# Kernel optimization log

Hardware: AMD Instinct MI355X
Metric: run time of the kernel (lower is better)

## Reference

```python
import jax, jax.numpy as jnp
import numpy as np

FP8_MAX = 448.0  # e4m3fn max
ACT_EPS = 1e-4
W_EPS = 1e-6
BLK = 128


def quant_dequant_act_1x128(x):
    # x: [E, M, K]. One scale per (row, 128-col) tile; scale = max(|x|, eps)/448.
    E, M, K = x.shape
    xb = x.reshape(E, M, K // BLK, BLK)
    amax = jnp.max(jnp.abs(xb), axis=-1, keepdims=True)
    safe = jnp.maximum(amax, ACT_EPS)
    q = (xb * (FP8_MAX / safe)).astype(jnp.float8_e4m3fn)
    return (q.astype(jnp.float32) * (safe / FP8_MAX)).reshape(E, M, K)


def quant_dequant_weight_128x128(w):
    # w: [E, N, K]. One scale per 128x128 block; scale = max(|w|, eps)/448.
    E, N, K = w.shape
    wb = w.reshape(E, N // BLK, BLK, K // BLK, BLK)
    amax = jnp.max(jnp.abs(wb), axis=(2, 4), keepdims=True)
    safe = jnp.maximum(amax, W_EPS)
    q = (wb * (FP8_MAX / safe)).astype(jnp.float8_e4m3fn)
    return (q.astype(jnp.float32) * (safe / FP8_MAX)).reshape(E, N, K)


def setup_inputs() -> dict:
    key = jax.random.key(0)
    kx, kw = jax.random.split(key)
    E, M, K, N = 8, 4096, 2048, 2048
    x = jax.random.normal(kx, (E, M, K), dtype=jnp.float32)
    weight = jax.random.normal(kw, (E, N, K), dtype=jnp.float32) * 0.02
    return {"x": x, "weight": weight}


def reference(x, weight):
    # fp8 blockwise quantize both operands, then grouped GEMM per expert.
    xq = quant_dequant_act_1x128(x)          # [E, M, K]
    wq = quant_dequant_weight_128x128(weight)  # [E, N, K]
    return jnp.einsum('emk,enk->emn', xq, wq)  # [E, M, N]
```

## Files before the change

kernel.cpp:

```cpp
#include <hip/hip_runtime.h>

typedef float f32x4 __attribute__((ext_vector_type(4)));

static constexpr int E_ = 8, M_ = 4096, K_ = 2048, N_ = 2048;
static constexpr int KB_ = K_ / 128;
static constexpr int MT_ = M_ / 128;
static constexpr int NT_ = N_ / 128;
#define FP8MAX 448.0f

__global__ __launch_bounds__(256) void quant_x_kernel(const float* __restrict__ x,
                                                      unsigned char* __restrict__ qx,
                                                      float* __restrict__ sx) {
  long tile = (long)blockIdx.x * 8 + (threadIdx.x >> 5);
  int lane = threadIdx.x & 31;
  f32x4 v = *(const f32x4*)(x + tile * 128 + lane * 4);
  float am = fmaxf(fmaxf(fabsf(v[0]), fabsf(v[1])), fmaxf(fabsf(v[2]), fabsf(v[3])));
#pragma unroll
  for (int off = 16; off; off >>= 1) am = fmaxf(am, __shfl_xor(am, off, 32));
  float safe = fmaxf(am, 1e-4f);
  float qs = FP8MAX / safe;
  int pk = 0;
  pk = __builtin_amdgcn_cvt_pk_fp8_f32(v[0] * qs, v[1] * qs, pk, false);
  pk = __builtin_amdgcn_cvt_pk_fp8_f32(v[2] * qs, v[3] * qs, pk, true);
  *(int*)(qx + tile * 128 + lane * 4) = pk;
  if (lane == 0) sx[tile] = safe / FP8MAX;
}

__global__ __launch_bounds__(256) void quant_w_kernel(const float* __restrict__ w,
                                                      unsigned char* __restrict__ qw,
                                                      float* __restrict__ sw) {
  int b = blockIdx.x;
  int kb = b % KB_;
  int t2 = b / KB_;
  int nb = t2 % NT_;
  int e = t2 / NT_;
  int tid = threadIdx.x;
  int r = tid >> 1;
  int c0 = (tid & 1) * 64;
  const float* base = w + ((long)(e * N_ + nb * 128 + r)) * K_ + kb * 128 + c0;
  f32x4 v[16];
  float am = 0.f;
#pragma unroll
  for (int j = 0; j < 16; ++j) {
    v[j] = *(const f32x4*)(base + j * 4);
    am = fmaxf(am, fmaxf(fmaxf(fabsf(v[j][0]), fabsf(v[j][1])),
                         fmaxf(fabsf(v[j][2]), fabsf(v[j][3]))));
  }
#pragma unroll
  for (int off = 32; off; off >>= 1) am = fmaxf(am, __shfl_xor(am, off, 64));
  __shared__ float red[4];
  if ((tid & 63) == 0) red[tid >> 6] = am;
  __syncthreads();
  am = fmaxf(fmaxf(red[0], red[1]), fmaxf(red[2], red[3]));
  float safe = fmaxf(am, 1e-6f);
  float qs = FP8MAX / safe;
  unsigned char* outp = qw + ((long)(e * N_ + nb * 128 + r)) * K_ + kb * 128 + c0;
#pragma unroll
  for (int j4 = 0; j4 < 4; ++j4) {
    uint4 pkv;
    unsigned int* pp = (unsigned int*)&pkv;
#pragma unroll
    for (int q = 0; q < 4; ++q) {
      int j = j4 * 4 + q;
      int pk = 0;
      pk = __builtin_amdgcn_cvt_pk_fp8_f32(v[j][0] * qs, v[j][1] * qs, pk, false);
      pk = __builtin_amdgcn_cvt_pk_fp8_f32(v[j][2] * qs, v[j][3] * qs, pk, true);
      pp[q] = (unsigned int)pk;
    }
    *(uint4*)(outp + j4 * 16) = pkv;
  }
  if (tid == 0) sw[(e * NT_ + nb) * KB_ + kb] = safe / FP8MAX;
}

__device__ inline void gload_lds16(const void* g, void* l) {
  __builtin_amdgcn_global_load_lds(
      (const __attribute__((address_space(1))) unsigned int*)g,
      (__attribute__((address_space(3))) unsigned int*)l, 16, 0, 0);
}

__global__ __launch_bounds__(256, 2) void gemm_kernel(
    const unsigned char* __restrict__ qx, const unsigned char* __restrict__ qw,
    const float* __restrict__ sx, const float* __restrict__ sw,
    float* __restrict__ out) {
  __shared__ unsigned char As[128 * 128];
  __shared__ unsigned char Bs[128 * 128];
  __shared__ float sxl[128][17];
  __shared__ float swl[16];

  const int e = blockIdx.y;
  const int mt = blockIdx.x / NT_;
  const int nt = blockIdx.x % NT_;
  const int brow = mt * 128, bcol = nt * 128;
  const int tid = threadIdx.x;
  const int w = tid >> 6, l = tid & 63;
  const int wr = w >> 1, wc = w & 1;
  const int qq = l >> 4, rl = l & 15;

  {
    int row = tid >> 1, half = (tid & 1) * 8;
    const float* sp = sx + ((long)(e * M_ + brow + row)) * KB_ + half;
    f32x4 s0 = *(const f32x4*)sp;
    f32x4 s1 = *(const f32x4*)(sp + 4);
#pragma unroll
    for (int j = 0; j < 4; ++j) {
      sxl[row][half + j] = s0[j];
      sxl[row][half + 4 + j] = s1[j];
    }
    if (tid < KB_) swl[tid] = sw[(e * NT_ + nt) * KB_ + tid];
  }

  f32x4 acc[4][4] = {};

  const unsigned char* Ab = qx + (long)(e * M_ + brow) * K_;
  const unsigned char* Bb = qw + (long)(e * N_ + bcol) * K_;
  const int lr8 = l >> 3, lc8 = l & 7;
  const int sch = (lc8 ^ lr8) * 16;
  const int o8 = (qq & 1) * 8;
  const int ch = qq >> 1;

  for (int kb = 0; kb < KB_; ++kb) {
    __syncthreads();
#pragma unroll
    for (int i = 0; i < 4; ++i) {
      const int rt = i * 32 + w * 8;
      gload_lds16(Ab + (long)(rt + lr8) * K_ + kb * 128 + sch, As + rt * 128);
      gload_lds16(Bb + (long)(rt + lr8) * K_ + kb * 128 + sch, Bs + rt * 128);
    }
    __syncthreads();

    long af[4][4], bf[4][4];
#pragma unroll
    for (int f = 0; f < 4; ++f) {
      const int ra = wr * 64 + f * 16 + rl;
      const int rb = wc * 64 + f * 16 + rl;
      const int rxa = ra & 7, rxb = rb & 7;
#pragma unroll
      for (int ks = 0; ks < 4; ++ks) {
        const int c = ks * 2 + ch;
        af[f][ks] = *(const long*)(As + ra * 128 + ((c ^ rxa) * 16) + o8);
        bf[f][ks] = *(const long*)(Bs + rb * 128 + ((c ^ rxb) * 16) + o8);
      }
    }

    const float swk = swl[kb];
    float sxs[4][4];
#pragma unroll
    for (int mf = 0; mf < 4; ++mf)
#pragma unroll
      for (int r = 0; r < 4; ++r)
        sxs[mf][r] = sxl[wr * 64 + mf * 16 + qq * 4 + r][kb] * swk;

#pragma unroll
    for (int mf = 0; mf < 4; ++mf)
#pragma unroll
      for (int nf = 0; nf < 4; ++nf) {
        f32x4 p = {0.f, 0.f, 0.f, 0.f};
#pragma unroll
        for (int ks = 0; ks < 4; ++ks)
          p = __builtin_amdgcn_mfma_f32_16x16x32_fp8_fp8(af[mf][ks], bf[nf][ks], p, 0, 0, 0);
#pragma unroll
        for (int r = 0; r < 4; ++r) acc[mf][nf][r] += p[r] * sxs[mf][r];
      }
  }

#pragma unroll
  for (int mf = 0; mf < 4; ++mf) {
    const int m = brow + wr * 64 + mf * 16 + qq * 4;
#pragma unroll
    for (int nf = 0; nf < 4; ++nf) {
      const int n = bcol + wc * 64 + nf * 16 + rl;
      float* op = out + ((long)(e * M_ + m)) * N_ + n;
#pragma unroll
      for (int r = 0; r < 4; ++r) op[(long)r * N_] = acc[mf][nf][r];
    }
  }
}

extern "C" void kernel_launch(void* const* d_in, const int* in_sizes, int n_in,
                              void* d_out, int out_size, void* d_ws, size_t ws_size,
                              hipStream_t stream) {
  const float* x = (const float*)d_in[0];
  const float* wt = (const float*)d_in[1];
  float* out = (float*)d_out;

  unsigned char* ws = (unsigned char*)d_ws;
  unsigned char* qx = ws;
  unsigned char* qw = ws + (size_t)E_ * M_ * K_;
  float* sx = (float*)(qw + (size_t)E_ * N_ * K_);
  float* sw = sx + (size_t)E_ * M_ * KB_;

  quant_x_kernel<<<dim3((E_ * M_ * KB_) / 8), dim3(256), 0, stream>>>(x, qx, sx);
  quant_w_kernel<<<dim3(E_ * NT_ * KB_), dim3(256), 0, stream>>>(wt, qw, sw);
  gemm_kernel<<<dim3(MT_ * NT_, E_), dim3(256), 0, stream>>>(qx, qw, sx, sw, out);
}
```

Baseline: 403.8 us.

## Rework fp8 GEMM into 256x256 double-buffered pipelined tiles with 512 threads

The GEMM kernel now uses 256x256 output tiles with 8 waves and double-buffered LDS for A and B. Global-to-LDS loads for step k+2 are interleaved with the MFMA phases of the current step, fenced by explicit barriers and vmcnt waits. It also adds a swizzled block order for L2 locality, s_setprio around the MFMA bursts, and a transposed scale layout read as vectors. The aim is to hide load latency and raise reuse per byte loaded. In exchange, LDS use rises to about 144KB per block, which limits each CU to one block, and the hand-written wait and barrier schedule is fragile.

```diff
diff --git a/kernel.cpp b/kernel.cpp
--- a/kernel.cpp
+++ b/kernel.cpp
@@ -3,9 +3,12 @@
 typedef float f32x4 __attribute__((ext_vector_type(4)));
 
 static constexpr int E_ = 8, M_ = 4096, K_ = 2048, N_ = 2048;
-static constexpr int KB_ = K_ / 128;
-static constexpr int MT_ = M_ / 128;
-static constexpr int NT_ = N_ / 128;
+static constexpr int KB_ = 16;
+static constexpr int NB128 = N_ / 128;
+static constexpr int BM = 256, BN = 256, BK = 128;
+static constexpr int KT = K_ / BK;
+static constexpr int MT2 = M_ / BM;
+static constexpr int NT2 = N_ / BN;
 #define FP8MAX 448.0f
 
 __global__ __launch_bounds__(256) void quant_x_kernel(const float* __restrict__ x,
@@ -32,8 +35,8 @@
   int b = blockIdx.x;
   int kb = b % KB_;
   int t2 = b / KB_;
-  int nb = t2 % NT_;
-  int e = t2 / NT_;
+  int nb = t2 % NB128;
+  int e = t2 / NB128;
   int tid = threadIdx.x;
   int r = tid >> 1;
   int c0 = (tid & 1) * 64;
@@ -69,109 +72,162 @@
     }
     *(uint4*)(outp + j4 * 16) = pkv;
   }
-  if (tid == 0) sw[(e * NT_ + nb) * KB_ + kb] = safe / FP8MAX;
-}
-
-__device__ inline void gload_lds16(const void* g, void* l) {
+  if (tid == 0) sw[(e * NB128 + nb) * KB_ + kb] = safe / FP8MAX;
+}
+
+__device__ inline void gload16(const void* g, void* l) {
   __builtin_amdgcn_global_load_lds(
       (const __attribute__((address_space(1))) unsigned int*)g,
       (__attribute__((address_space(3))) unsigned int*)l, 16, 0, 0);
 }
 
-__global__ __launch_bounds__(256, 2) void gemm_kernel(
+#define BAR __builtin_amdgcn_s_barrier()
+
+#define LOAD_A(MFH)                                                             \
+  _Pragma("unroll") for (int mf = 0; mf < 4; ++mf) {                            \
+    _Pragma("unroll") for (int ks = 0; ks < 4; ++ks)                            \
+      af[mf][ks] = *(const long*)&Acur[(arow0 + (MFH) * 64 + mf * 16) * BK +    \
+                                       cofs[ks]];                               \
+  }
+
+#define LOAD_B(NF0)                                                             \
+  _Pragma("unroll") for (int nf2 = 0; nf2 < 2; ++nf2) {                         \
+    _Pragma("unroll") for (int ks = 0; ks < 4; ++ks)                            \
+      bf[(NF0) + nf2][ks] =                                                     \
+          *(const long*)&Bcur[(brow0 + ((NF0) + nf2) * 16) * BK + cofs[ks]];    \
+  }
+
+#define LOAD_SXW(MFH)                                                           \
+  _Pragma("unroll") for (int mf = 0; mf < 4; ++mf)                              \
+      sxw[mf] = (*(const f32x4*)&sxl[kt][wr * 128 + (MFH) * 64 + mf * 16 +      \
+                                         qq * 4]) * swk;
+
+#define MFMA_FOLD(MFH, NF0)                                                     \
+  do {                                                                          \
+    __builtin_amdgcn_s_setprio(1);                                              \
+    _Pragma("unroll") for (int mf = 0; mf < 4; ++mf) {                          \
+      _Pragma("unroll") for (int nf2 = 0; nf2 < 2; ++nf2) {                     \
+        f32x4 p = {0.f, 0.f, 0.f, 0.f};                                         \
+        _Pragma("unroll") for (int ks = 0; ks < 4; ++ks)                        \
+            p = __builtin_amdgcn_mfma_f32_16x16x32_fp8_fp8(                     \
+                af[mf][ks], bf[(NF0) + nf2][ks], p, 0, 0, 0);                   \
+        _Pragma("unroll") for (int r = 0; r < 4; ++r)                           \
+            acc[(MFH) * 4 + mf][(NF0) + nf2][r] += p[r] * sxw[mf][r];           \
+      }                                                                         \
+    }                                                                           \
+    __builtin_amdgcn_s_setprio(0);                                              \
+  } while (0)
+
+__global__ __launch_bounds__(512, 2) void gemm_kernel(
     const unsigned char* __restrict__ qx, const unsigned char* __restrict__ qw,
     const float* __restrict__ sx, const float* __restrict__ sw,
     float* __restrict__ out) {
-  __shared__ unsigned char As[128 * 128];
-  __shared__ unsigned char Bs[128 * 128];
-  __shared__ float sxl[128][17];
-  __shared__ float swl[16];
+  __shared__ unsigned char As[2][BM * BK];
+  __shared__ unsigned char Bs[2][BN * BK];
+  __shared__ float sxl[KT][BM];
+  __shared__ float swl[2][KT];
 
   const int e = blockIdx.y;
-  const int mt = blockIdx.x / NT_;
-  const int nt = blockIdx.x % NT_;
-  const int brow = mt * 128, bcol = nt * 128;
+  const int x = blockIdx.x;
+  const int swz = (x & 7) * 16 + (x >> 3);
+  const int mt = swz >> 3, nt = swz & 7;
+  const int brow = mt * BM, bcol = nt * BN;
+
   const int tid = threadIdx.x;
   const int w = tid >> 6, l = tid & 63;
-  const int wr = w >> 1, wc = w & 1;
+  const int wr = w >> 2, wc = w & 3;
   const int qq = l >> 4, rl = l & 15;
+  const int o8 = (qq & 1) * 8, ch = qq >> 1;
+  const int rx = rl & 7;
+
+  const unsigned char* Ab = qx + (size_t)(e * M_ + brow) * K_;
+  const unsigned char* Bb = qw + (size_t)(e * N_ + bcol) * K_;
 
   {
-    int row = tid >> 1, half = (tid & 1) * 8;
-    const float* sp = sx + ((long)(e * M_ + brow + row)) * KB_ + half;
+    int row = tid >> 1, h = (tid & 1) * 8;
+    const float* sp = sx + (size_t)(e * M_ + brow + row) * KB_ + h;
     f32x4 s0 = *(const f32x4*)sp;
     f32x4 s1 = *(const f32x4*)(sp + 4);
 #pragma unroll
     for (int j = 0; j < 4; ++j) {
-      sxl[row][half + j] = s0[j];
-      sxl[row][half + 4 + j] = s1[j];
+      sxl[h + j][row] = s0[j];
+      sxl[h + 4 + j][row] = s1[j];
     }
-    if (tid < KB_) swl[tid] = sw[(e * NT_ + nt) * KB_ + tid];
-  }
-
-  f32x4 acc[4][4] = {};
-
-  const unsigned char* Ab = qx + (long)(e * M_ + brow) * K_;
-  const unsigned char* Bb = qw + (long)(e * N_ + bcol) * K_;
-  const int lr8 = l >> 3, lc8 = l & 7;
-  const int sch = (lc8 ^ lr8) * 16;
-  const int o8 = (qq & 1) * 8;
-  const int ch = qq >> 1;
-
-  for (int kb = 0; kb < KB_; ++kb) {
-    __syncthreads();
-#pragma unroll
-    for (int i = 0; i < 4; ++i) {
-      const int rt = i * 32 + w * 8;
-      gload_lds16(Ab + (long)(rt + lr8) * K_ + kb * 128 + sch, As + rt * 128);
-      gload_lds16(Bb + (long)(rt + lr8) * K_ + kb * 128 + sch, Bs + rt * 128);
-    }
-    __syncthreads();
-
-    long af[4][4], bf[4][4];
-#pragma unroll
-    for (int f = 0; f < 4; ++f) {
-      const int ra = wr * 64 + f * 16 + rl;
-      const int rb = wc * 64 + f * 16 + rl;
-      const int rxa = ra & 7, rxb = rb & 7;
-#pragma unroll
-      for (int ks = 0; ks < 4; ++ks) {
-        const int c = ks * 2 + ch;
-        af[f][ks] = *(const long*)(As + ra * 128 + ((c ^ rxa) * 16) + o8);
-        bf[f][ks] = *(const long*)(Bs + rb * 128 + ((c ^ rxb) * 16) + o8);
-      }
-    }
-
-    const float swk = swl[kb];
-    float sxs[4][4];
-#pragma unroll
-    for (int mf = 0; mf < 4; ++mf)
-#pragma unroll
-      for (int r = 0; r < 4; ++r)
-        sxs[mf][r] = sxl[wr * 64 + mf * 16 + qq * 4 + r][kb] * swk;
-
-#pragma unroll
-    for (int mf = 0; mf < 4; ++mf)
-#pragma unroll
-      for (int nf = 0; nf < 4; ++nf) {
-        f32x4 p = {0.f, 0.f, 0.f, 0.f};
-#pragma unroll
-        for (int ks = 0; ks < 4; ++ks)
-          p = __builtin_amdgcn_mfma_f32_16x16x32_fp8_fp8(af[mf][ks], bf[nf][ks], p, 0, 0, 0);
-#pragma unroll
-        for (int r = 0; r < 4; ++r) acc[mf][nf][r] += p[r] * sxs[mf][r];
-      }
-  }
-
-#pragma unroll
-  for (int mf = 0; mf < 4; ++mf) {
-    const int m = brow + wr * 64 + mf * 16 + qq * 4;
+    if (tid < 32)
+      swl[tid >> 4][tid & 15] =
+          sw[(e * NB128 + nt * 2 + (tid >> 4)) * KB_ + (tid & 15)];
+  }
+  __syncthreads();
+
+  const int c8 = l & 7, r8 = (l >> 3) & 7;
+  const int srcswz = (c8 ^ r8) * 16;
+  auto stageA = [&](int rowbase, int kt2, int tb) {
+    gload16(Ab + (size_t)(rowbase + w * 8 + (l >> 3)) * K_ + kt2 * BK + srcswz,
+            &As[tb][(rowbase + w * 8) * BK]);
+  };
+  auto stageB = [&](int rowbase0, int kt2, int tb) {
+    int rb = rowbase0 + (w & 3) * 8 + (w >> 2) * 64;
+    gload16(Bb + (size_t)(rb + (l >> 3)) * K_ + kt2 * BK + srcswz,
+            &Bs[tb][rb * BK]);
+  };
+
+#pragma unroll
+  for (int t = 0; t < 2; ++t) {
+    stageA(0, t, t); stageA(128, t, t); stageA(64, t, t); stageA(192, t, t);
+    stageB(0, t, t); stageB(128, t, t); stageB(32, t, t); stageB(160, t, t);
+  }
+  asm volatile("s_waitcnt vmcnt(8)" ::: "memory");
+  BAR;
+  __builtin_amdgcn_sched_barrier(0);
+
+  f32x4 acc[8][4] = {};
+  long af[4][4], bf[4][4];
+  f32x4 sxw[4];
+  int cofs[4];
+#pragma unroll
+  for (int ks = 0; ks < 4; ++ks) cofs[ks] = (((2 * ks + ch) ^ rx) * 16) + o8;
+  const int arow0 = wr * 128 + rl;
+  const int brow0 = wc * 64 + rl;
+
+  for (int kt = 0; kt < KT; ++kt) {
+    const int buf = kt & 1;
+    const unsigned char* Acur = As[buf];
+    const unsigned char* Bcur = Bs[buf];
+    const float swk = swl[wc >> 1][kt];
+
+    LOAD_A(0); LOAD_B(0); LOAD_SXW(0);
+    BAR;
+    MFMA_FOLD(0, 0);
+    BAR;
+    if (kt + 2 < KT) { stageA(0, kt + 2, buf); stageA(128, kt + 2, buf); }
+    LOAD_B(2);
+    BAR;
+    MFMA_FOLD(0, 2);
+    BAR;
+    if (kt + 2 < KT) { stageB(0, kt + 2, buf); stageB(128, kt + 2, buf); }
+    LOAD_A(1); LOAD_SXW(1);
+    BAR;
+    MFMA_FOLD(1, 0);
+    BAR;
+    if (kt + 2 < KT) { stageB(32, kt + 2, buf); stageB(160, kt + 2, buf);
+                       stageA(64, kt + 2, buf); stageA(192, kt + 2, buf); }
+    BAR;
+    MFMA_FOLD(1, 2);
+    if (kt < KT - 2)       { asm volatile("s_waitcnt vmcnt(8)" ::: "memory"); }
+    else if (kt == KT - 2) { asm volatile("s_waitcnt vmcnt(0)" ::: "memory"); }
+    BAR;
+    __builtin_amdgcn_sched_barrier(0);
+  }
+
+#pragma unroll
+  for (int MF = 0; MF < 8; ++MF) {
+    const int m = brow + wr * 128 + MF * 16 + qq * 4;
 #pragma unroll
     for (int nf = 0; nf < 4; ++nf) {
       const int n = bcol + wc * 64 + nf * 16 + rl;
-      float* op = out + ((long)(e * M_ + m)) * N_ + n;
-#pragma unroll
-      for (int r = 0; r < 4; ++r) op[(long)r * N_] = acc[mf][nf][r];
+      float* op = out + (size_t)(e * M_ + m) * N_ + n;
+#pragma unroll
+      for (int r = 0; r < 4; ++r) op[(size_t)r * N_] = acc[MF][nf][r];
     }
   }
 }
@@ -190,6 +246,6 @@
   float* sw = sx + (size_t)E_ * M_ * KB_;
 
   quant_x_kernel<<<dim3((E_ * M_ * KB_) / 8), dim3(256), 0, stream>>>(x, qx, sx);
-  quant_w_kernel<<<dim3(E_ * NT_ * KB_), dim3(256), 0, stream>>>(wt, qw, sw);
-  gemm_kernel<<<dim3(MT_ * NT_, E_), dim3(256), 0, stream>>>(qx, qw, sx, sw, out);
-}
+  quant_w_kernel<<<dim3(E_ * NB128 * KB_), dim3(256), 0, stream>>>(wt, qw, sw);
+  gemm_kernel<<<dim3(MT2 * NT2, E_), dim3(512), 0, stream>>>(qx, qw, sx, sw, out);
+}
```

After: 1.202 ms. 2.98x slower.

## Dequantize to bf16 upfront and run a 256x256 double-buffered bf16 GEMM

Applied to the files above, without the earlier changes.

Quantization kernels now round to fp8 and immediately dequantize into bf16 buffers, so the GEMM needs no per-block scale multiplies and can accumulate directly in MFMA. The new GEMM uses 256x256 tiles with 512 threads, double-buffered LDS loads interleaved with MFMA quads, setprio and a tile swizzle. This doubles operand bytes read and uses bf16 MFMA, which has lower peak throughput than fp8. The old fp8 path is kept as a fallback when workspace is too small.

```diff
diff --git a/kernel.cpp b/kernel.cpp
--- a/kernel.cpp
+++ b/kernel.cpp
@@ -1,16 +1,222 @@
 #include <hip/hip_runtime.h>
 
 typedef float f32x4 __attribute__((ext_vector_type(4)));
+typedef float f32x2 __attribute__((ext_vector_type(2)));
+typedef short s16x8 __attribute__((ext_vector_type(8)));
 
 static constexpr int E_ = 8, M_ = 4096, K_ = 2048, N_ = 2048;
-static constexpr int KB_ = K_ / 128;
-static constexpr int MT_ = M_ / 128;
-static constexpr int NT_ = N_ / 128;
+static constexpr int KB_ = 16;
+static constexpr int NB128 = N_ / 128;
 #define FP8MAX 448.0f
 
-__global__ __launch_bounds__(256) void quant_x_kernel(const float* __restrict__ x,
-                                                      unsigned char* __restrict__ qx,
-                                                      float* __restrict__ sx) {
+__device__ inline unsigned short f2bf(float f) {
+  unsigned u = __builtin_bit_cast(unsigned, f);
+  return (unsigned short)((u + 0x7FFFu + ((u >> 16) & 1u)) >> 16);
+}
+
+
+__global__ __launch_bounds__(256) void quant_x_bf16(const float* __restrict__ x,
+                                                    unsigned short* __restrict__ qxb) {
+  long tile = (long)blockIdx.x * 8 + (threadIdx.x >> 5);
+  int lane = threadIdx.x & 31;
+  f32x4 v = *(const f32x4*)(x + tile * 128 + lane * 4);
+  float am = fmaxf(fmaxf(fabsf(v[0]), fabsf(v[1])), fmaxf(fabsf(v[2]), fabsf(v[3])));
+#pragma unroll
+  for (int off = 16; off; off >>= 1) am = fmaxf(am, __shfl_xor(am, off, 32));
+  float safe = fmaxf(am, 1e-4f);
+  float qs = FP8MAX / safe, ds = safe / FP8MAX;
+  int pk = 0;
+  pk = __builtin_amdgcn_cvt_pk_fp8_f32(v[0] * qs, v[1] * qs, pk, false);
+  pk = __builtin_amdgcn_cvt_pk_fp8_f32(v[2] * qs, v[3] * qs, pk, true);
+  f32x2 lo = __builtin_amdgcn_cvt_pk_f32_fp8(pk, false);
+  f32x2 hi = __builtin_amdgcn_cvt_pk_f32_fp8(pk, true);
+  ushort4 o;
+  o.x = f2bf(lo[0] * ds); o.y = f2bf(lo[1] * ds);
+  o.z = f2bf(hi[0] * ds); o.w = f2bf(hi[1] * ds);
+  *(ushort4*)(qxb + tile * 128 + lane * 4) = o;
+}
+
+__global__ __launch_bounds__(256) void quant_w_bf16(const float* __restrict__ w,
+                                                    unsigned short* __restrict__ qwb) {
+  int b = blockIdx.x;
+  int kb = b % KB_;
+  int t2 = b / KB_;
+  int nb = t2 % NB128;
+  int e = t2 / NB128;
+  int tid = threadIdx.x;
+  int r = tid >> 1;
+  int c0 = (tid & 1) * 64;
+  const float* base = w + ((long)(e * N_ + nb * 128 + r)) * K_ + kb * 128 + c0;
+  f32x4 v[16];
+  float am = 0.f;
+#pragma unroll
+  for (int j = 0; j < 16; ++j) {
+    v[j] = *(const f32x4*)(base + j * 4);
+    am = fmaxf(am, fmaxf(fmaxf(fabsf(v[j][0]), fabsf(v[j][1])),
+                         fmaxf(fabsf(v[j][2]), fabsf(v[j][3]))));
+  }
+#pragma unroll
+  for (int off = 32; off; off >>= 1) am = fmaxf(am, __shfl_xor(am, off, 64));
+  __shared__ float red[4];
+  if ((tid & 63) == 0) red[tid >> 6] = am;
+  __syncthreads();
+  am = fmaxf(fmaxf(red[0], red[1]), fmaxf(red[2], red[3]));
+  float safe = fmaxf(am, 1e-6f);
+  float qs = FP8MAX / safe, ds = safe / FP8MAX;
+  unsigned short* outp = qwb + ((long)(e * N_ + nb * 128 + r)) * K_ + kb * 128 + c0;
+#pragma unroll
+  for (int j2 = 0; j2 < 8; ++j2) {
+    ushort4 o[2];
+#pragma unroll
+    for (int h = 0; h < 2; ++h) {
+      int j = j2 * 2 + h;
+      int pk = 0;
+      pk = __builtin_amdgcn_cvt_pk_fp8_f32(v[j][0] * qs, v[j][1] * qs, pk, false);
+      pk = __builtin_amdgcn_cvt_pk_fp8_f32(v[j][2] * qs, v[j][3] * qs, pk, true);
+      f32x2 lo = __builtin_amdgcn_cvt_pk_f32_fp8(pk, false);
+      f32x2 hi = __builtin_amdgcn_cvt_pk_f32_fp8(pk, true);
+      o[h].x = f2bf(lo[0] * ds); o[h].y = f2bf(lo[1] * ds);
+      o[h].z = f2bf(hi[0] * ds); o[h].w = f2bf(hi[1] * ds);
+    }
+    ushort4* dst = (ushort4*)(outp + j2 * 8);
+    dst[0] = o[0]; dst[1] = o[1];
+  }
+}
+
+__device__ inline void gload16(const void* g, void* l) {
+  __builtin_amdgcn_global_load_lds(
+      (const __attribute__((address_space(1))) unsigned int*)g,
+      (__attribute__((address_space(3))) unsigned int*)l, 16, 0, 0);
+}
+
+#define BAR __builtin_amdgcn_s_barrier()
+
+#define QUAD(AV, BV, MO, NO)                                                    \
+  do {                                                                          \
+    __builtin_amdgcn_s_setprio(1);                                              \
+    _Pragma("unroll") for (int mf = 0; mf < 4; ++mf)                            \
+      _Pragma("unroll") for (int nf = 0; nf < 2; ++nf) {                        \
+        acc[(MO) + mf][(NO) + nf] = __builtin_amdgcn_mfma_f32_16x16x32_bf16(    \
+            AV[mf][0], BV[nf][0], acc[(MO) + mf][(NO) + nf], 0, 0, 0);          \
+        acc[(MO) + mf][(NO) + nf] = __builtin_amdgcn_mfma_f32_16x16x32_bf16(    \
+            AV[mf][1], BV[nf][1], acc[(MO) + mf][(NO) + nf], 0, 0, 0);          \
+      }                                                                         \
+    __builtin_amdgcn_s_setprio(0);                                              \
+  } while (0)
+
+static constexpr int GKT = 32;
+
+__global__ __launch_bounds__(512, 2) void gemm_bf16(
+    const unsigned short* __restrict__ qxb, const unsigned short* __restrict__ qwb,
+    float* __restrict__ out) {
+  __shared__ unsigned char As[2][256 * 128];
+  __shared__ unsigned char Bs[2][256 * 128];
+
+  const int e = blockIdx.y;
+  const int x = blockIdx.x;
+  const int swz = (x & 7) * 16 + (x >> 3);
+  const int mt = swz >> 3, nt = swz & 7;
+  const int brow = mt * 256, bcol = nt * 256;
+
+  const int tid = threadIdx.x;
+  const int w = tid >> 6, l = tid & 63;
+  const int wr = w >> 2, wc = w & 3;
+  const int qq = l >> 4, rl = l & 15;
+
+  const unsigned char* Ab = (const unsigned char*)(qxb + (size_t)(e * M_ + brow) * K_);
+  const unsigned char* Bb = (const unsigned char*)(qwb + (size_t)(e * N_ + bcol) * K_);
+
+  const int gsw = (((l & 7) ^ ((l >> 3) & 7)) << 4);
+  auto stA = [&](int u, int t2, int tb) {
+    const int r = u * 64 + w * 8 + (l >> 3);
+    gload16(Ab + (size_t)r * (K_ * 2) + t2 * 128 + gsw, &As[tb][(u * 64 + w * 8) * 128]);
+  };
+  auto stB = [&](int u, int t2, int tb) {
+    const int r = u * 64 + w * 8 + (l >> 3);
+    gload16(Bb + (size_t)r * (K_ * 2) + t2 * 128 + gsw, &Bs[tb][(u * 64 + w * 8) * 128]);
+  };
+
+#pragma unroll
+  for (int t = 0; t < 2; ++t) {
+    stA(0, t, t); stA(1, t, t); stA(2, t, t); stA(3, t, t);
+    stB(0, t, t); stB(1, t, t); stB(2, t, t); stB(3, t, t);
+  }
+  asm volatile("s_waitcnt vmcnt(8)" ::: "memory");
+  BAR;
+  __builtin_amdgcn_sched_barrier(0);
+
+  f32x4 acc[8][4] = {};
+  int cofs[2];
+#pragma unroll
+  for (int ks = 0; ks < 2; ++ks) cofs[ks] = (((ks * 4 + qq) ^ (rl & 7)) << 4);
+  const int aro = wr * 64 + rl;
+  const int bro = wc * 64 + rl;
+
+  s16x8 af[4][2], ag[4][2], bf[2][2], bg[2][2];
+
+  for (int kt = 0; kt < GKT; ++kt) {
+    const int buf = kt & 1;
+    const unsigned char* Acur = As[buf];
+    const unsigned char* Bcur = Bs[buf];
+
+#pragma unroll
+    for (int mf = 0; mf < 4; ++mf)
+#pragma unroll
+      for (int ks = 0; ks < 2; ++ks)
+        af[mf][ks] = *(const s16x8*)&Acur[(aro + mf * 16) * 128 + cofs[ks]];
+#pragma unroll
+    for (int nf = 0; nf < 2; ++nf)
+#pragma unroll
+      for (int ks = 0; ks < 2; ++ks)
+        bf[nf][ks] = *(const s16x8*)&Bcur[(bro + nf * 16) * 128 + cofs[ks]];
+    BAR;
+    QUAD(af, bf, 0, 0);
+    BAR;
+    if (kt + 2 < GKT) { stA(0, kt + 2, buf); stA(1, kt + 2, buf); }
+#pragma unroll
+    for (int nf = 0; nf < 2; ++nf)
+#pragma unroll
+      for (int ks = 0; ks < 2; ++ks)
+        bg[nf][ks] = *(const s16x8*)&Bcur[(bro + 32 + nf * 16) * 128 + cofs[ks]];
+    BAR;
+    QUAD(af, bg, 0, 2);
+    BAR;
+    if (kt + 2 < GKT) { stB(0, kt + 2, buf); stB(1, kt + 2, buf);
+                        stB(2, kt + 2, buf); stB(3, kt + 2, buf); }
+#pragma unroll
+    for (int mf = 0; mf < 4; ++mf)
+#pragma unroll
+      for (int ks = 0; ks < 2; ++ks)
+        ag[mf][ks] = *(const s16x8*)&Acur[(aro + 128 + mf * 16) * 128 + cofs[ks]];
+    BAR;
+    QUAD(ag, bf, 4, 0);
+    BAR;
+    if (kt + 2 < GKT) { stA(2, kt + 2, buf); stA(3, kt + 2, buf); }
+    BAR;
+    QUAD(ag, bg, 4, 2);
+    if (kt < GKT - 2)       { asm volatile("s_waitcnt vmcnt(8)" ::: "memory"); }
+    else if (kt == GKT - 2) { asm volatile("s_waitcnt vmcnt(0)" ::: "memory"); }
+    BAR;
+    __builtin_amdgcn_sched_barrier(0);
+  }
+
+#pragma unroll
+  for (int MF = 0; MF < 8; ++MF) {
+    const int m = brow + (MF >> 2) * 128 + wr * 64 + (MF & 3) * 16 + qq * 4;
+#pragma unroll
+    for (int nfq = 0; nfq < 4; ++nfq) {
+      const int n = bcol + wc * 64 + (nfq >> 1) * 32 + (nfq & 1) * 16 + rl;
+      float* op = out + (size_t)(e * M_ + m) * N_ + n;
+#pragma unroll
+      for (int r = 0; r < 4; ++r) op[(size_t)r * N_] = acc[MF][nfq][r];
+    }
+  }
+}
+
+
+__global__ __launch_bounds__(256) void quant_x_fb(const float* __restrict__ x,
+                                                  unsigned char* __restrict__ qx,
+                                                  float* __restrict__ sx) {
   long tile = (long)blockIdx.x * 8 + (threadIdx.x >> 5);
   int lane = threadIdx.x & 31;
   f32x4 v = *(const f32x4*)(x + tile * 128 + lane * 4);
@@ -26,14 +232,14 @@
   if (lane == 0) sx[tile] = safe / FP8MAX;
 }
 
-__global__ __launch_bounds__(256) void quant_w_kernel(const float* __restrict__ w,
-                                                      unsigned char* __restrict__ qw,
-                                                      float* __restrict__ sw) {
+__global__ __launch_bounds__(256) void quant_w_fb(const float* __restrict__ w,
+                                                  unsigned char* __restrict__ qw,
+                                                  float* __restrict__ sw) {
   int b = blockIdx.x;
   int kb = b % KB_;
   int t2 = b / KB_;
-  int nb = t2 % NT_;
-  int e = t2 / NT_;
+  int nb = t2 % NB128;
+  int e = t2 / NB128;
   int tid = threadIdx.x;
   int r = tid >> 1;
   int c0 = (tid & 1) * 64;
@@ -69,27 +275,22 @@
     }
     *(uint4*)(outp + j4 * 16) = pkv;
   }
-  if (tid == 0) sw[(e * NT_ + nb) * KB_ + kb] = safe / FP8MAX;
-}
-
-__device__ inline void gload_lds16(const void* g, void* l) {
-  __builtin_amdgcn_global_load_lds(
-      (const __attribute__((address_space(1))) unsigned int*)g,
-      (__attribute__((address_space(3))) unsigned int*)l, 16, 0, 0);
-}
-
-__global__ __launch_bounds__(256, 2) void gemm_kernel(
+  if (tid == 0) sw[(e * NB128 + nb) * KB_ + kb] = safe / FP8MAX;
+}
+
+__global__ __launch_bounds__(256, 2) void gemm_fb(
     const unsigned char* __restrict__ qx, const unsigned char* __restrict__ qw,
     const float* __restrict__ sx, const float* __restrict__ sw,
     float* __restrict__ out) {
-  __shared__ unsigned char As[128 * 128];
-  __shared__ unsigned char Bs[128 * 128];
+  __shared__ unsigned char Asf[128 * 128];
+  __shared__ unsigned char Bsf[128 * 128];
   __shared__ float sxl[128][17];
   __shared__ float swl[16];
 
+  const int NTf = N_ / 128;
   const int e = blockIdx.y;
-  const int mt = blockIdx.x / NT_;
-  const int nt = blockIdx.x % NT_;
+  const int mt = blockIdx.x / NTf;
+  const int nt = blockIdx.x % NTf;
   const int brow = mt * 128, bcol = nt * 128;
   const int tid = threadIdx.x;
   const int w = tid >> 6, l = tid & 63;
@@ -106,11 +307,10 @@
       sxl[row][half + j] = s0[j];
       sxl[row][half + 4 + j] = s1[j];
     }
-    if (tid < KB_) swl[tid] = sw[(e * NT_ + nt) * KB_ + tid];
+    if (tid < KB_) swl[tid] = sw[(e * NTf + nt) * KB_ + tid];
   }
 
   f32x4 acc[4][4] = {};
-
   const unsigned char* Ab = qx + (long)(e * M_ + brow) * K_;
   const unsigned char* Bb = qw + (long)(e * N_ + bcol) * K_;
   const int lr8 = l >> 3, lc8 = l & 7;
@@ -123,12 +323,12 @@
 #pragma unroll
     for (int i = 0; i < 4; ++i) {
       const int rt = i * 32 + w * 8;
-      gload_lds16(Ab + (long)(rt + lr8) * K_ + kb * 128 + sch, As + rt * 128);
-      gload_lds16(Bb + (long)(rt + lr8) * K_ + kb * 128 + sch, Bs + rt * 128);
+      gload16(Ab + (long)(rt + lr8) * K_ + kb * 128 + sch, Asf + rt * 128);
+      gload16(Bb + (long)(rt + lr8) * K_ + kb * 128 + sch, Bsf + rt * 128);
     }
     __syncthreads();
 
-    long af[4][4], bf[4][4];
+    long af[4][4], bfr[4][4];
 #pragma unroll
     for (int f = 0; f < 4; ++f) {
       const int ra = wr * 64 + f * 16 + rl;
@@ -137,8 +337,8 @@
 #pragma unroll
       for (int ks = 0; ks < 4; ++ks) {
         const int c = ks * 2 + ch;
-        af[f][ks] = *(const long*)(As + ra * 128 + ((c ^ rxa) * 16) + o8);
-        bf[f][ks] = *(const long*)(Bs + rb * 128 + ((c ^ rxb) * 16) + o8);
+        af[f][ks] = *(const long*)(Asf + ra * 128 + ((c ^ rxa) * 16) + o8);
+        bfr[f][ks] = *(const long*)(Bsf + rb * 128 + ((c ^ rxb) * 16) + o8);
       }
     }
 
@@ -157,7 +357,7 @@
         f32x4 p = {0.f, 0.f, 0.f, 0.f};
 #pragma unroll
         for (int ks = 0; ks < 4; ++ks)
-          p = __builtin_amdgcn_mfma_f32_16x16x32_fp8_fp8(af[mf][ks], bf[nf][ks], p, 0, 0, 0);
+          p = __builtin_amdgcn_mfma_f32_16x16x32_fp8_fp8(af[mf][ks], bfr[nf][ks], p, 0, 0, 0);
 #pragma unroll
         for (int r = 0; r < 4; ++r) acc[mf][nf][r] += p[r] * sxs[mf][r];
       }
@@ -183,13 +383,21 @@
   const float* wt = (const float*)d_in[1];
   float* out = (float*)d_out;
 
-  unsigned char* ws = (unsigned char*)d_ws;
-  unsigned char* qx = ws;
-  unsigned char* qw = ws + (size_t)E_ * M_ * K_;
-  float* sx = (float*)(qw + (size_t)E_ * N_ * K_);
-  float* sw = sx + (size_t)E_ * M_ * KB_;
-
-  quant_x_kernel<<<dim3((E_ * M_ * KB_) / 8), dim3(256), 0, stream>>>(x, qx, sx);
-  quant_w_kernel<<<dim3(E_ * NT_ * KB_), dim3(256), 0, stream>>>(wt, qw, sw);
-  gemm_kernel<<<dim3(MT_ * NT_, E_), dim3(256), 0, stream>>>(qx, qw, sx, sw, out);
-}
+  const size_t needed = ((size_t)E_ * M_ * K_ + (size_t)E_ * N_ * K_) * 2;
+  if (ws_size >= needed) {
+    unsigned short* qxb = (unsigned short*)d_ws;
+    unsigned short* qwb = qxb + (size_t)E_ * M_ * K_;
+    quant_x_bf16<<<dim3((E_ * M_ * KB_) / 8), dim3(256), 0, stream>>>(x, qxb);
+    quant_w_bf16<<<dim3(E_ * NB128 * KB_), dim3(256), 0, stream>>>(wt, qwb);
+    gemm_bf16<<<dim3((M_ / 256) * (N_ / 256), E_), dim3(512), 0, stream>>>(qxb, qwb, out);
+  } else {
+    unsigned char* ws = (unsigned char*)d_ws;
+    unsigned char* qx = ws;
+    unsigned char* qw = ws + (size_t)E_ * M_ * K_;
+    float* sx = (float*)(qw + (size_t)E_ * N_ * K_);
+    float* sw = sx + (size_t)E_ * M_ * KB_;
+    quant_x_fb<<<dim3((E_ * M_ * KB_) / 8), dim3(256), 0, stream>>>(x, qx, sx);
+    quant_w_fb<<<dim3(E_ * NB128 * KB_), dim3(256), 0, stream>>>(wt, qw, sw);
+    gemm_fb<<<dim3((M_ / 128) * (N_ / 128), E_), dim3(256), 0, stream>>>(qx, qw, sx, sw, out);
+  }
+}
```

Result: slower. 422.1 us (+4.5%).
